# Performance work log

Hardware: AMD Instinct MI355X
Metric: run time of the kernel (lower is better)

The kernel has to match this reference:

```python
import jax, jax.numpy as jnp
import numpy as np

ROUTING_ITERS = 3
EPS = 1e-8

def squash(s):
    # standard CapsNet squash along last axis
    sq = jnp.sum(s * s, axis=-1, keepdims=True)
    return s * (sq / (1.0 + sq)) / jnp.sqrt(sq + EPS)

def setup_inputs() -> dict:
    key = jax.random.key(0)
    k1, k2 = jax.random.split(key)
    B, N_IN, D_IN = 64, 2048, 16
    N_OUT, D_OUT = 32, 32
    x = jax.random.normal(k1, (B, N_IN, D_IN), dtype=jnp.float32)
    kernel = jax.random.normal(k2, (N_IN, N_OUT, D_IN, D_OUT), dtype=jnp.float32) * 0.05
    return {"x": x, "kernel": kernel}

def reference(x, kernel):
    # U[b,n,j,d] = sum_k x[b,n,k] * kernel[n,j,k,d]  (per-input-capsule transform)
    U = jnp.einsum('bnk,njkd->bnjd', x, kernel)
    b, n_in, n_out, _ = U.shape
    Blog = jnp.zeros((b, n_in, n_out), dtype=U.dtype)
    V = None
    for i in range(ROUTING_ITERS):
        C = jax.nn.softmax(Blog, axis=-1)            # [b, n_in, n_out]
        S = jnp.einsum('bnj,bnjd->bjd', C, U)        # weighted sum over input capsules
        V = squash(S)                                # [b, n_out, d_out]
        if i != ROUTING_ITERS - 1:                   # last B update is dead code in original
            Blog = Blog + jnp.einsum('bnjd,bjd->bnj', U, V)
    return V
```

## Files before the change

kernel.cpp:

```cpp
#include <hip/hip_runtime.h>


#define NIN   2048
#define DIN   16
#define NOUT  32
#define DOUT  32
#define NTILE 16
#define NB    (NIN/NTILE)

typedef __attribute__((ext_vector_type(8)))  short s16x8;
typedef __attribute__((ext_vector_type(16))) float f32x16;

#define WS_BLOG   0
#define WS_SPART  4194304
#define WS_SPART2 12582912
#define WS_V      13107200
#define WS_KTF    13172736
#define WS_XTF    29949952

__device__ __forceinline__ unsigned short f2bf(float f) {
  unsigned u = __float_as_uint(f);
  u = (u + 0x7fffu + ((u >> 16) & 1u)) >> 16;
  return (unsigned short)u;
}

__global__ __launch_bounds__(256) void conv_k(const float* __restrict__ Kr,
                                              unsigned short* __restrict__ Ktf) {
  const int n = blockIdx.x;
  const int t = threadIdx.x;
  __shared__ float kl[16384];
  const float* src = Kr + (size_t)n * 16384;
#pragma unroll
  for (int c = 0; c < 16; ++c) {
    const int idx = (c * 256 + t) * 4;
    const int jj  = idx >> 9;
    const int sidx = (idx & ~28) | (((((idx >> 2) & 7) ^ (jj & 7))) << 2);
    *(float4*)&kl[sidx] = *(const float4*)(src + idx);
  }
  __syncthreads();
  unsigned short* dst = Ktf + (size_t)n * 16384;
#pragma unroll
  for (int c = 0; c < 8; ++c) {
    const int chunk = c * 256 + t;
    const int d = chunk >> 6, lane = chunk & 63;
    const int j = lane & 31, khi = lane >> 5;
    const int dsw = ((((d >> 2) ^ (j & 7)) << 2)) | (d & 3);
    unsigned short u8[8];
#pragma unroll
    for (int i = 0; i < 8; ++i)
      u8[i] = f2bf(kl[j * 512 + (khi * 8 + i) * 32 + dsw]);
    uint4 o;
    o.x = u8[0] | ((unsigned)u8[1] << 16);
    o.y = u8[2] | ((unsigned)u8[3] << 16);
    o.z = u8[4] | ((unsigned)u8[5] << 16);
    o.w = u8[6] | ((unsigned)u8[7] << 16);
    *(uint4*)(dst + (size_t)chunk * 8) = o;
  }
}

__global__ __launch_bounds__(256) void conv_x(const float* __restrict__ x,
                                              unsigned short* __restrict__ xtf) {
  const int g = blockIdx.x * 256 + threadIdx.x;
  const int bh = g >> 17, rem = g & 131071;
  const int n = rem >> 6, lane = rem & 63;
  const int b = bh * 32 + (lane & 31), khi = lane >> 5;
  const float* src = x + ((size_t)b * NIN + n) * DIN + khi * 8;
  unsigned short u8[8];
#pragma unroll
  for (int i = 0; i < 8; ++i) u8[i] = f2bf(src[i]);
  uint4 o;
  o.x = u8[0] | ((unsigned)u8[1] << 16);
  o.y = u8[2] | ((unsigned)u8[3] << 16);
  o.z = u8[4] | ((unsigned)u8[5] << 16);
  o.w = u8[6] | ((unsigned)u8[7] << 16);
  *(uint4*)(xtf + (size_t)g * 8) = o;
}

template<int MODE>
__global__ __launch_bounds__(512, 2) void caps_mfma(
    const unsigned short* __restrict__ Ktf, const unsigned short* __restrict__ xtf,
    const float* __restrict__ Vin, float* __restrict__ Blog,
    float* __restrict__ Spart)
{
  const int tid = threadIdx.x;
  const int w = tid >> 6, lane = tid & 63;
  const int j = lane & 31, hi = lane >> 5;
  const int nt = blockIdx.x, bh = blockIdx.y;
  const int n0 = nt * NTILE;

  __shared__ float Ds[8][32][32];
  __shared__ float Cs[32][32];

  float sacc[16][4];
#pragma unroll
  for (int r = 0; r < 16; ++r)
#pragma unroll
    for (int dd = 0; dd < 4; ++dd) sacc[r][dd] = 0.f;

  float vreg[16][4];
  if (MODE != 0) {
#pragma unroll
    for (int r = 0; r < 16; ++r) {
      const int b = (r & 3) + 4 * hi + 8 * (r >> 2);
      const float4 v4 = *(const float4*)(Vin + (((size_t)(bh * 32 + b) * 32 + j) * 32 + w * 4));
      vreg[r][0] = v4.x; vreg[r][1] = v4.y; vreg[r][2] = v4.z; vreg[r][3] = v4.w;
    }
  }

  const int rb = tid >> 5;
  const int rj = tid & 31;

  const unsigned short* xp = xtf + (((size_t)bh * NIN + n0) * 64 + lane) * 8;
  const unsigned short* kp = Ktf + (((size_t)n0 * 32 + w * 4) * 64 + lane) * 8;

  s16x8 a = *(const s16x8*)xp;
  s16x8 bf[4];
#pragma unroll
  for (int dd = 0; dd < 4; ++dd) bf[dd] = *(const s16x8*)(kp + dd * 512);

#pragma unroll 1
  for (int nn = 0; nn < NTILE; ++nn) {
    const int n = n0 + nn;

    f32x16 u[4];
#pragma unroll
    for (int dd = 0; dd < 4; ++dd) {
      f32x16 z;
#pragma unroll
      for (int q = 0; q < 16; ++q) z[q] = 0.f;
      u[dd] = __builtin_amdgcn_mfma_f32_32x32x16_bf16(a, bf[dd], z, 0, 0, 0);
    }

    const int inc = (nn < NTILE - 1) ? 1 : 0;
    const s16x8 a2 = *(const s16x8*)(xp + inc * 512);
    s16x8 bf2[4];
#pragma unroll
    for (int dd = 0; dd < 4; ++dd)
      bf2[dd] = *(const s16x8*)(kp + inc * 16384 + dd * 512);
    xp += inc * 512;
    kp += inc * 16384;

    if (MODE == 0) {
#pragma unroll
      for (int r = 0; r < 16; ++r)
#pragma unroll
        for (int dd = 0; dd < 4; ++dd)
          sacc[r][dd] = fmaf(0.03125f, u[dd][r], sacc[r][dd]);
    } else {
#pragma unroll
      for (int r = 0; r < 16; ++r) {
        const float pd = u[0][r] * vreg[r][0] + u[1][r] * vreg[r][1]
                       + u[2][r] * vreg[r][2] + u[3][r] * vreg[r][3];
        const int b = (r & 3) + 4 * hi + 8 * (r >> 2);
        Ds[w][b][j] = pd;
      }
      __syncthreads();
      float l0 = 0.f, l1 = 0.f;
#pragma unroll
      for (int ww = 0; ww < 8; ++ww) { l0 += Ds[ww][rb][rj]; l1 += Ds[ww][rb + 16][rj]; }
      const size_t bi0 = ((size_t)(bh * 32 + rb) * NIN + n) * 32 + rj;
      const size_t bi1 = ((size_t)(bh * 32 + rb + 16) * NIN + n) * 32 + rj;
      if (MODE == 1) { Blog[bi0] = l0; Blog[bi1] = l1; }
      else           { l0 += Blog[bi0]; l1 += Blog[bi1]; }
      const float e0 = __expf(l0), e1 = __expf(l1);
      float s0 = e0, s1 = e1;
#pragma unroll
      for (int mm = 16; mm >= 1; mm >>= 1) {
        s0 += __shfl_xor(s0, mm, 64);
        s1 += __shfl_xor(s1, mm, 64);
      }
      Cs[rb][rj]      = __fdividef(e0, s0);
      Cs[rb + 16][rj] = __fdividef(e1, s1);
      __syncthreads();
#pragma unroll
      for (int r = 0; r < 16; ++r) {
        const int b = (r & 3) + 4 * hi + 8 * (r >> 2);
        const float c = Cs[b][j];
#pragma unroll
        for (int dd = 0; dd < 4; ++dd) sacc[r][dd] = fmaf(c, u[dd][r], sacc[r][dd]);
      }
    }

    a = a2;
#pragma unroll
    for (int dd = 0; dd < 4; ++dd) bf[dd] = bf2[dd];
  }

  float* Sp = Spart + (size_t)(bh * NB + nt) * 32768;
#pragma unroll
  for (int r = 0; r < 16; ++r) {
    const int b = (r & 3) + 4 * hi + 8 * (r >> 2);
    *(float4*)(Sp + ((size_t)b * 32 + j) * 32 + w * 4) =
        make_float4(sacc[r][0], sacc[r][1], sacc[r][2], sacc[r][3]);
  }
}

__global__ __launch_bounds__(256) void reduce_s1(const float* __restrict__ Spart,
                                                 float* __restrict__ Spart2) {
  const int g = blockIdx.x * 256 + threadIdx.x;
  const int e = g & 65535, p = g >> 16;
  const int bh = e >> 15, ei = e & 32767;
  const float* base = Spart + ((size_t)(bh * NB + p * 16)) * 32768 + ei;
  float s = 0.f;
#pragma unroll
  for (int i = 0; i < 16; ++i) s += base[(size_t)i * 32768];
  Spart2[(size_t)p * 65536 + e] = s;
}

__global__ __launch_bounds__(256) void reduce_s2(const float* __restrict__ Spart2,
                                                 float* __restrict__ Vout) {
  const int t = blockIdx.x * 256 + threadIdx.x;
  float s = 0.f;
#pragma unroll
  for (int p = 0; p < 8; ++p) s += Spart2[(size_t)p * 65536 + t];
  float sq = s * s;
#pragma unroll
  for (int m = 16; m >= 1; m >>= 1) sq += __shfl_xor(sq, m, 64);
  Vout[t] = s * (sq / (1.0f + sq)) * rsqrtf(sq + 1e-8f);
}

extern "C" void kernel_launch(void* const* d_in, const int* in_sizes, int n_in,
                              void* d_out, int out_size, void* d_ws, size_t ws_size,
                              hipStream_t stream) {
  const float* x  = (const float*)d_in[0];
  const float* Kr = (const float*)d_in[1];
  float* ws = (float*)d_ws;
  float* Blog   = ws + WS_BLOG;
  float* Spart  = ws + WS_SPART;
  float* Spart2 = ws + WS_SPART2;
  float* V      = ws + WS_V;
  unsigned short* Ktf = (unsigned short*)(ws + WS_KTF);
  unsigned short* xtf = (unsigned short*)(ws + WS_XTF);
  float* out = (float*)d_out;

  conv_k<<<NIN, 256, 0, stream>>>(Kr, Ktf);
  conv_x<<<1024, 256, 0, stream>>>(x, xtf);

  const dim3 g(NB, 2), blk(512);
  caps_mfma<0><<<g, blk, 0, stream>>>(Ktf, xtf, nullptr, Blog, Spart);
  reduce_s1<<<2048, 256, 0, stream>>>(Spart, Spart2);
  reduce_s2<<<256, 256, 0, stream>>>(Spart2, V);
  caps_mfma<1><<<g, blk, 0, stream>>>(Ktf, xtf, V, Blog, Spart);
  reduce_s1<<<2048, 256, 0, stream>>>(Spart, Spart2);
  reduce_s2<<<256, 256, 0, stream>>>(Spart2, V);
  caps_mfma<2><<<g, blk, 0, stream>>>(Ktf, xtf, V, Blog, Spart);
  reduce_s1<<<2048, 256, 0, stream>>>(Spart, Spart2);
  reduce_s2<<<256, 256, 0, stream>>>(Spart2, out);
}
```

Before: 360.4 us.

## Fuse routing iterations and reductions into one cooperative persistent kernel

Replaces the nine per-iteration launches (three MFMA kernels plus two-stage reductions) with a single cooperative kernel. It loops over the three routing iterations and uses grid-wide syncs to separate the partial-S write from the reduce-and-squash step. This removes launch gaps and the intermediate Spart2 buffer. In exchange, only 64K threads out of 131K do the 128-deep strided reduction, the grid barriers add cost, and the design relies on all 256 blocks of 512 threads being co-resident.

```diff
diff --git a/kernel.cpp b/kernel.cpp
--- a/kernel.cpp
+++ b/kernel.cpp
@@ -1,4 +1,7 @@
 #include <hip/hip_runtime.h>
+#include <hip/hip_cooperative_groups.h>
+
+namespace cg = cooperative_groups;
 
 
 #define NIN   2048
@@ -13,10 +16,9 @@
 
 #define WS_BLOG   0
 #define WS_SPART  4194304
-#define WS_SPART2 12582912
-#define WS_V      13107200
-#define WS_KTF    13172736
-#define WS_XTF    29949952
+#define WS_V      12582912
+#define WS_KTF    12648448
+#define WS_XTF    29425664
 
 __device__ __forceinline__ unsigned short f2bf(float f) {
   unsigned u = __float_as_uint(f);
@@ -76,147 +78,146 @@
   *(uint4*)(xtf + (size_t)g * 8) = o;
 }
 
-template<int MODE>
-__global__ __launch_bounds__(512, 2) void caps_mfma(
+__global__ __launch_bounds__(512, 2) void caps_persist(
     const unsigned short* __restrict__ Ktf, const unsigned short* __restrict__ xtf,
-    const float* __restrict__ Vin, float* __restrict__ Blog,
-    float* __restrict__ Spart)
+    float* __restrict__ Blog, float* __restrict__ Spart,
+    float* __restrict__ Vbuf, float* __restrict__ Out)
 {
+  cg::grid_group grid = cg::this_grid();
   const int tid = threadIdx.x;
   const int w = tid >> 6, lane = tid & 63;
   const int j = lane & 31, hi = lane >> 5;
-  const int nt = blockIdx.x, bh = blockIdx.y;
+  const int blk = blockIdx.x;
+  const int nt = blk & 127, bh = blk >> 7;
   const int n0 = nt * NTILE;
 
   __shared__ float Ds[8][32][32];
   __shared__ float Cs[32][32];
 
-  float sacc[16][4];
-#pragma unroll
-  for (int r = 0; r < 16; ++r)
-#pragma unroll
-    for (int dd = 0; dd < 4; ++dd) sacc[r][dd] = 0.f;
-
-  float vreg[16][4];
-  if (MODE != 0) {
+  const int rb = tid >> 5;
+  const int rj = tid & 31;
+  const int gtid = blk * 512 + tid;
+
+#pragma unroll 1
+  for (int it = 0; it < 3; ++it) {
+    float sacc[16][4];
+#pragma unroll
+    for (int r = 0; r < 16; ++r)
+#pragma unroll
+      for (int dd = 0; dd < 4; ++dd) sacc[r][dd] = 0.f;
+
+    float vreg[16][4];
+    if (it != 0) {
+#pragma unroll
+      for (int r = 0; r < 16; ++r) {
+        const int b = (r & 3) + 4 * hi + 8 * (r >> 2);
+        const float4 v4 = *(const float4*)(Vbuf + (((size_t)(bh * 32 + b) * 32 + j) * 32 + w * 4));
+        vreg[r][0] = v4.x; vreg[r][1] = v4.y; vreg[r][2] = v4.z; vreg[r][3] = v4.w;
+      }
+    }
+
+    const unsigned short* xp = xtf + (((size_t)bh * NIN + n0) * 64 + lane) * 8;
+    const unsigned short* kp = Ktf + (((size_t)n0 * 32 + w * 4) * 64 + lane) * 8;
+
+    s16x8 a = *(const s16x8*)xp;
+    s16x8 bf[4];
+#pragma unroll
+    for (int dd = 0; dd < 4; ++dd) bf[dd] = *(const s16x8*)(kp + dd * 512);
+
+#pragma unroll 1
+    for (int nn = 0; nn < NTILE; ++nn) {
+      const int n = n0 + nn;
+
+      f32x16 u[4];
+#pragma unroll
+      for (int dd = 0; dd < 4; ++dd) {
+        f32x16 z;
+#pragma unroll
+        for (int q = 0; q < 16; ++q) z[q] = 0.f;
+        u[dd] = __builtin_amdgcn_mfma_f32_32x32x16_bf16(a, bf[dd], z, 0, 0, 0);
+      }
+
+      const int inc = (nn < NTILE - 1) ? 1 : 0;
+      const s16x8 a2 = *(const s16x8*)(xp + inc * 512);
+      s16x8 bf2[4];
+#pragma unroll
+      for (int dd = 0; dd < 4; ++dd)
+        bf2[dd] = *(const s16x8*)(kp + inc * 16384 + dd * 512);
+      xp += inc * 512;
+      kp += inc * 16384;
+
+      if (it == 0) {
+#pragma unroll
+        for (int r = 0; r < 16; ++r)
+#pragma unroll
+          for (int dd = 0; dd < 4; ++dd)
+            sacc[r][dd] = fmaf(0.03125f, u[dd][r], sacc[r][dd]);
+      } else {
+#pragma unroll
+        for (int r = 0; r < 16; ++r) {
+          const float pd = u[0][r] * vreg[r][0] + u[1][r] * vreg[r][1]
+                         + u[2][r] * vreg[r][2] + u[3][r] * vreg[r][3];
+          const int b = (r & 3) + 4 * hi + 8 * (r >> 2);
+          Ds[w][b][j] = pd;
+        }
+        __syncthreads();
+        float l0 = 0.f, l1 = 0.f;
+#pragma unroll
+        for (int ww = 0; ww < 8; ++ww) { l0 += Ds[ww][rb][rj]; l1 += Ds[ww][rb + 16][rj]; }
+        const size_t bi0 = ((size_t)(bh * 32 + rb) * NIN + n) * 32 + rj;
+        const size_t bi1 = ((size_t)(bh * 32 + rb + 16) * NIN + n) * 32 + rj;
+        if (it == 1) { Blog[bi0] = l0; Blog[bi1] = l1; }
+        else         { l0 += Blog[bi0]; l1 += Blog[bi1]; }
+        const float e0 = __expf(l0), e1 = __expf(l1);
+        float s0 = e0, s1 = e1;
+#pragma unroll
+        for (int mm = 16; mm >= 1; mm >>= 1) {
+          s0 += __shfl_xor(s0, mm, 64);
+          s1 += __shfl_xor(s1, mm, 64);
+        }
+        Cs[rb][rj]      = __fdividef(e0, s0);
+        Cs[rb + 16][rj] = __fdividef(e1, s1);
+        __syncthreads();
+#pragma unroll
+        for (int r = 0; r < 16; ++r) {
+          const int b = (r & 3) + 4 * hi + 8 * (r >> 2);
+          const float c = Cs[b][j];
+#pragma unroll
+          for (int dd = 0; dd < 4; ++dd) sacc[r][dd] = fmaf(c, u[dd][r], sacc[r][dd]);
+        }
+      }
+
+      a = a2;
+#pragma unroll
+      for (int dd = 0; dd < 4; ++dd) bf[dd] = bf2[dd];
+    }
+
+    float* Sp = Spart + (size_t)blk * 32768;
 #pragma unroll
     for (int r = 0; r < 16; ++r) {
       const int b = (r & 3) + 4 * hi + 8 * (r >> 2);
-      const float4 v4 = *(const float4*)(Vin + (((size_t)(bh * 32 + b) * 32 + j) * 32 + w * 4));
-      vreg[r][0] = v4.x; vreg[r][1] = v4.y; vreg[r][2] = v4.z; vreg[r][3] = v4.w;
-    }
+      *(float4*)(Sp + ((size_t)b * 32 + j) * 32 + w * 4) =
+          make_float4(sacc[r][0], sacc[r][1], sacc[r][2], sacc[r][3]);
+    }
+
+    grid.sync();
+
+    if (gtid < 65536) {
+      const int bhe = gtid >> 15;
+      const int ei  = gtid & 32767;
+      const float* base = Spart + (size_t)(bhe * NB) * 32768 + ei;
+      float s = 0.f;
+#pragma unroll 8
+      for (int t = 0; t < NB; ++t) s += base[(size_t)t * 32768];
+      float sq = s * s;
+#pragma unroll
+      for (int m = 16; m >= 1; m >>= 1) sq += __shfl_xor(sq, m, 64);
+      const float v = s * (sq / (1.0f + sq)) * rsqrtf(sq + 1e-8f);
+      if (it < 2) Vbuf[gtid] = v;
+      else        Out[gtid]  = v;
+    }
+    if (it < 2) grid.sync();
   }
-
-  const int rb = tid >> 5;
-  const int rj = tid & 31;
-
-  const unsigned short* xp = xtf + (((size_t)bh * NIN + n0) * 64 + lane) * 8;
-  const unsigned short* kp = Ktf + (((size_t)n0 * 32 + w * 4) * 64 + lane) * 8;
-
-  s16x8 a = *(const s16x8*)xp;
-  s16x8 bf[4];
-#pragma unroll
-  for (int dd = 0; dd < 4; ++dd) bf[dd] = *(const s16x8*)(kp + dd * 512);
-
-#pragma unroll 1
-  for (int nn = 0; nn < NTILE; ++nn) {
-    const int n = n0 + nn;
-
-    f32x16 u[4];
-#pragma unroll
-    for (int dd = 0; dd < 4; ++dd) {
-      f32x16 z;
-#pragma unroll
-      for (int q = 0; q < 16; ++q) z[q] = 0.f;
-      u[dd] = __builtin_amdgcn_mfma_f32_32x32x16_bf16(a, bf[dd], z, 0, 0, 0);
-    }
-
-    const int inc = (nn < NTILE - 1) ? 1 : 0;
-    const s16x8 a2 = *(const s16x8*)(xp + inc * 512);
-    s16x8 bf2[4];
-#pragma unroll
-    for (int dd = 0; dd < 4; ++dd)
-      bf2[dd] = *(const s16x8*)(kp + inc * 16384 + dd * 512);
-    xp += inc * 512;
-    kp += inc * 16384;
-
-    if (MODE == 0) {
-#pragma unroll
-      for (int r = 0; r < 16; ++r)
-#pragma unroll
-        for (int dd = 0; dd < 4; ++dd)
-          sacc[r][dd] = fmaf(0.03125f, u[dd][r], sacc[r][dd]);
-    } else {
-#pragma unroll
-      for (int r = 0; r < 16; ++r) {
-        const float pd = u[0][r] * vreg[r][0] + u[1][r] * vreg[r][1]
-                       + u[2][r] * vreg[r][2] + u[3][r] * vreg[r][3];
-        const int b = (r & 3) + 4 * hi + 8 * (r >> 2);
-        Ds[w][b][j] = pd;
-      }
-      __syncthreads();
-      float l0 = 0.f, l1 = 0.f;
-#pragma unroll
-      for (int ww = 0; ww < 8; ++ww) { l0 += Ds[ww][rb][rj]; l1 += Ds[ww][rb + 16][rj]; }
-      const size_t bi0 = ((size_t)(bh * 32 + rb) * NIN + n) * 32 + rj;
-      const size_t bi1 = ((size_t)(bh * 32 + rb + 16) * NIN + n) * 32 + rj;
-      if (MODE == 1) { Blog[bi0] = l0; Blog[bi1] = l1; }
-      else           { l0 += Blog[bi0]; l1 += Blog[bi1]; }
-      const float e0 = __expf(l0), e1 = __expf(l1);
-      float s0 = e0, s1 = e1;
-#pragma unroll
-      for (int mm = 16; mm >= 1; mm >>= 1) {
-        s0 += __shfl_xor(s0, mm, 64);
-        s1 += __shfl_xor(s1, mm, 64);
-      }
-      Cs[rb][rj]      = __fdividef(e0, s0);
-      Cs[rb + 16][rj] = __fdividef(e1, s1);
-      __syncthreads();
-#pragma unroll
-      for (int r = 0; r < 16; ++r) {
-        const int b = (r & 3) + 4 * hi + 8 * (r >> 2);
-        const float c = Cs[b][j];
-#pragma unroll
-        for (int dd = 0; dd < 4; ++dd) sacc[r][dd] = fmaf(c, u[dd][r], sacc[r][dd]);
-      }
-    }
-
-    a = a2;
-#pragma unroll
-    for (int dd = 0; dd < 4; ++dd) bf[dd] = bf2[dd];
-  }
-
-  float* Sp = Spart + (size_t)(bh * NB + nt) * 32768;
-#pragma unroll
-  for (int r = 0; r < 16; ++r) {
-    const int b = (r & 3) + 4 * hi + 8 * (r >> 2);
-    *(float4*)(Sp + ((size_t)b * 32 + j) * 32 + w * 4) =
-        make_float4(sacc[r][0], sacc[r][1], sacc[r][2], sacc[r][3]);
-  }
-}
-
-__global__ __launch_bounds__(256) void reduce_s1(const float* __restrict__ Spart,
-                                                 float* __restrict__ Spart2) {
-  const int g = blockIdx.x * 256 + threadIdx.x;
-  const int e = g & 65535, p = g >> 16;
-  const int bh = e >> 15, ei = e & 32767;
-  const float* base = Spart + ((size_t)(bh * NB + p * 16)) * 32768 + ei;
-  float s = 0.f;
-#pragma unroll
-  for (int i = 0; i < 16; ++i) s += base[(size_t)i * 32768];
-  Spart2[(size_t)p * 65536 + e] = s;
-}
-
-__global__ __launch_bounds__(256) void reduce_s2(const float* __restrict__ Spart2,
-                                                 float* __restrict__ Vout) {
-  const int t = blockIdx.x * 256 + threadIdx.x;
-  float s = 0.f;
-#pragma unroll
-  for (int p = 0; p < 8; ++p) s += Spart2[(size_t)p * 65536 + t];
-  float sq = s * s;
-#pragma unroll
-  for (int m = 16; m >= 1; m >>= 1) sq += __shfl_xor(sq, m, 64);
-  Vout[t] = s * (sq / (1.0f + sq)) * rsqrtf(sq + 1e-8f);
 }
 
 extern "C" void kernel_launch(void* const* d_in, const int* in_sizes, int n_in,
@@ -225,10 +226,9 @@
   const float* x  = (const float*)d_in[0];
   const float* Kr = (const float*)d_in[1];
   float* ws = (float*)d_ws;
-  float* Blog   = ws + WS_BLOG;
-  float* Spart  = ws + WS_SPART;
-  float* Spart2 = ws + WS_SPART2;
-  float* V      = ws + WS_V;
+  float* Blog  = ws + WS_BLOG;
+  float* Spart = ws + WS_SPART;
+  float* Vbuf  = ws + WS_V;
   unsigned short* Ktf = (unsigned short*)(ws + WS_KTF);
   unsigned short* xtf = (unsigned short*)(ws + WS_XTF);
   float* out = (float*)d_out;
@@ -236,14 +236,8 @@
   conv_k<<<NIN, 256, 0, stream>>>(Kr, Ktf);
   conv_x<<<1024, 256, 0, stream>>>(x, xtf);
 
-  const dim3 g(NB, 2), blk(512);
-  caps_mfma<0><<<g, blk, 0, stream>>>(Ktf, xtf, nullptr, Blog, Spart);
-  reduce_s1<<<2048, 256, 0, stream>>>(Spart, Spart2);
-  reduce_s2<<<256, 256, 0, stream>>>(Spart2, V);
-  caps_mfma<1><<<g, blk, 0, stream>>>(Ktf, xtf, V, Blog, Spart);
-  reduce_s1<<<2048, 256, 0, stream>>>(Spart, Spart2);
-  reduce_s2<<<256, 256, 0, stream>>>(Spart2, V);
-  caps_mfma<2><<<g, blk, 0, stream>>>(Ktf, xtf, V, Blog, Spart);
-  reduce_s1<<<2048, 256, 0, stream>>>(Spart, Spart2);
-  reduce_s2<<<256, 256, 0, stream>>>(Spart2, out);
-}
+  void* args[] = { (void*)&Ktf, (void*)&xtf, (void*)&Blog, (void*)&Spart,
+                   (void*)&Vbuf, (void*)&out };
+  hipLaunchCooperativeKernel((void*)caps_persist, dim3(256), dim3(512),
+                             args, 0, stream);
+}
```

Measured after the change: 675.5 us. 1.87x slower.

## Double-buffer MODE0 loads, remap block grid for L2 reuse, lighten barriers

Applied to the files above, without the earlier changes.

The MODE 0 kernel now keeps two independent load/MFMA streams (even and odd n), so global loads for one capsule overlap compute on the other. The 2D grid becomes a 1D grid where pairs of batch-halves sharing the same n tiles are adjacent, so both can reuse the same kernel weights from L2. The __syncthreads calls in the routing modes are replaced by a raw LDS waitcnt plus s_barrier with scheduling fences, which avoids waiting on outstanding global prefetches. The changes raise register pressure in MODE 0 and depend on the raw barrier sequence being correct.

```diff
diff --git a/kernel.cpp b/kernel.cpp
--- a/kernel.cpp
+++ b/kernel.cpp
@@ -22,6 +22,13 @@
   unsigned u = __float_as_uint(f);
   u = (u + 0x7fffu + ((u >> 16) & 1u)) >> 16;
   return (unsigned short)u;
+}
+
+__device__ __forceinline__ void lds_barrier() {
+  asm volatile("s_waitcnt lgkmcnt(0)" ::: "memory");
+  __builtin_amdgcn_sched_barrier(0);
+  __builtin_amdgcn_s_barrier();
+  __builtin_amdgcn_sched_barrier(0);
 }
 
 __global__ __launch_bounds__(256) void conv_k(const float* __restrict__ Kr,
@@ -85,7 +92,9 @@
   const int tid = threadIdx.x;
   const int w = tid >> 6, lane = tid & 63;
   const int j = lane & 31, hi = lane >> 5;
-  const int nt = blockIdx.x, bh = blockIdx.y;
+  const int blk = blockIdx.x;
+  const int nt = (blk >> 4) * 8 + (blk & 7);
+  const int bh = (blk >> 3) & 1;
   const int n0 = nt * NTILE;
 
   __shared__ float Ds[8][32][32];
@@ -97,56 +106,105 @@
 #pragma unroll
     for (int dd = 0; dd < 4; ++dd) sacc[r][dd] = 0.f;
 
-  float vreg[16][4];
-  if (MODE != 0) {
+  if (MODE == 0) {
+    const unsigned short* xpA = xtf + (((size_t)bh * NIN + n0) * 64 + lane) * 8;
+    const unsigned short* kpA = Ktf + (((size_t)n0 * 32 + w * 4) * 64 + lane) * 8;
+    const unsigned short* xpB = xpA + 512;
+    const unsigned short* kpB = kpA + 16384;
+
+    s16x8 aA = *(const s16x8*)xpA, aB = *(const s16x8*)xpB;
+    s16x8 bfA[4], bfB[4];
+#pragma unroll
+    for (int dd = 0; dd < 4; ++dd) {
+      bfA[dd] = *(const s16x8*)(kpA + dd * 512);
+      bfB[dd] = *(const s16x8*)(kpB + dd * 512);
+    }
+
+#pragma unroll 1
+    for (int nn = 0; nn < NTILE; nn += 2) {
+      f32x16 u[4];
+#pragma unroll
+      for (int dd = 0; dd < 4; ++dd) {
+        f32x16 z;
+#pragma unroll
+        for (int q = 0; q < 16; ++q) z[q] = 0.f;
+        u[dd] = __builtin_amdgcn_mfma_f32_32x32x16_bf16(aA, bfA[dd], z, 0, 0, 0);
+      }
+      {
+        const int inc = (nn + 2 < NTILE) ? 2 : 0;
+        xpA += inc * 512;  kpA += inc * 16384;
+        aA = *(const s16x8*)xpA;
+#pragma unroll
+        for (int dd = 0; dd < 4; ++dd) bfA[dd] = *(const s16x8*)(kpA + dd * 512);
+      }
+#pragma unroll
+      for (int r = 0; r < 16; ++r)
+#pragma unroll
+        for (int dd = 0; dd < 4; ++dd)
+          sacc[r][dd] = fmaf(0.03125f, u[dd][r], sacc[r][dd]);
+
+#pragma unroll
+      for (int dd = 0; dd < 4; ++dd) {
+        f32x16 z;
+#pragma unroll
+        for (int q = 0; q < 16; ++q) z[q] = 0.f;
+        u[dd] = __builtin_amdgcn_mfma_f32_32x32x16_bf16(aB, bfB[dd], z, 0, 0, 0);
+      }
+      {
+        const int inc = (nn + 3 < NTILE) ? 2 : 0;
+        xpB += inc * 512;  kpB += inc * 16384;
+        aB = *(const s16x8*)xpB;
+#pragma unroll
+        for (int dd = 0; dd < 4; ++dd) bfB[dd] = *(const s16x8*)(kpB + dd * 512);
+      }
+#pragma unroll
+      for (int r = 0; r < 16; ++r)
+#pragma unroll
+        for (int dd = 0; dd < 4; ++dd)
+          sacc[r][dd] = fmaf(0.03125f, u[dd][r], sacc[r][dd]);
+    }
+  } else {
+    float vreg[16][4];
 #pragma unroll
     for (int r = 0; r < 16; ++r) {
       const int b = (r & 3) + 4 * hi + 8 * (r >> 2);
       const float4 v4 = *(const float4*)(Vin + (((size_t)(bh * 32 + b) * 32 + j) * 32 + w * 4));
       vreg[r][0] = v4.x; vreg[r][1] = v4.y; vreg[r][2] = v4.z; vreg[r][3] = v4.w;
     }
-  }
-
-  const int rb = tid >> 5;
-  const int rj = tid & 31;
-
-  const unsigned short* xp = xtf + (((size_t)bh * NIN + n0) * 64 + lane) * 8;
-  const unsigned short* kp = Ktf + (((size_t)n0 * 32 + w * 4) * 64 + lane) * 8;
-
-  s16x8 a = *(const s16x8*)xp;
-  s16x8 bf[4];
-#pragma unroll
-  for (int dd = 0; dd < 4; ++dd) bf[dd] = *(const s16x8*)(kp + dd * 512);
+
+    const int rb = tid >> 5;
+    const int rj = tid & 31;
+
+    const unsigned short* xp = xtf + (((size_t)bh * NIN + n0) * 64 + lane) * 8;
+    const unsigned short* kp = Ktf + (((size_t)n0 * 32 + w * 4) * 64 + lane) * 8;
+
+    s16x8 a = *(const s16x8*)xp;
+    s16x8 bf[4];
+#pragma unroll
+    for (int dd = 0; dd < 4; ++dd) bf[dd] = *(const s16x8*)(kp + dd * 512);
 
 #pragma unroll 1
-  for (int nn = 0; nn < NTILE; ++nn) {
-    const int n = n0 + nn;
-
-    f32x16 u[4];
-#pragma unroll
-    for (int dd = 0; dd < 4; ++dd) {
-      f32x16 z;
-#pragma unroll
-      for (int q = 0; q < 16; ++q) z[q] = 0.f;
-      u[dd] = __builtin_amdgcn_mfma_f32_32x32x16_bf16(a, bf[dd], z, 0, 0, 0);
-    }
-
-    const int inc = (nn < NTILE - 1) ? 1 : 0;
-    const s16x8 a2 = *(const s16x8*)(xp + inc * 512);
-    s16x8 bf2[4];
-#pragma unroll
-    for (int dd = 0; dd < 4; ++dd)
-      bf2[dd] = *(const s16x8*)(kp + inc * 16384 + dd * 512);
-    xp += inc * 512;
-    kp += inc * 16384;
-
-    if (MODE == 0) {
-#pragma unroll
-      for (int r = 0; r < 16; ++r)
-#pragma unroll
-        for (int dd = 0; dd < 4; ++dd)
-          sacc[r][dd] = fmaf(0.03125f, u[dd][r], sacc[r][dd]);
-    } else {
+    for (int nn = 0; nn < NTILE; ++nn) {
+      const int n = n0 + nn;
+
+      f32x16 u[4];
+#pragma unroll
+      for (int dd = 0; dd < 4; ++dd) {
+        f32x16 z;
+#pragma unroll
+        for (int q = 0; q < 16; ++q) z[q] = 0.f;
+        u[dd] = __builtin_amdgcn_mfma_f32_32x32x16_bf16(a, bf[dd], z, 0, 0, 0);
+      }
+
+      const int inc = (nn < NTILE - 1) ? 1 : 0;
+      const s16x8 a2 = *(const s16x8*)(xp + inc * 512);
+      s16x8 bf2[4];
+#pragma unroll
+      for (int dd = 0; dd < 4; ++dd)
+        bf2[dd] = *(const s16x8*)(kp + inc * 16384 + dd * 512);
+      xp += inc * 512;
+      kp += inc * 16384;
+
 #pragma unroll
       for (int r = 0; r < 16; ++r) {
         const float pd = u[0][r] * vreg[r][0] + u[1][r] * vreg[r][1]
@@ -154,7 +212,7 @@
         const int b = (r & 3) + 4 * hi + 8 * (r >> 2);
         Ds[w][b][j] = pd;
       }
-      __syncthreads();
+      lds_barrier();
       float l0 = 0.f, l1 = 0.f;
 #pragma unroll
       for (int ww = 0; ww < 8; ++ww) { l0 += Ds[ww][rb][rj]; l1 += Ds[ww][rb + 16][rj]; }
@@ -171,7 +229,7 @@
       }
       Cs[rb][rj]      = __fdividef(e0, s0);
       Cs[rb + 16][rj] = __fdividef(e1, s1);
-      __syncthreads();
+      lds_barrier();
 #pragma unroll
       for (int r = 0; r < 16; ++r) {
         const int b = (r & 3) + 4 * hi + 8 * (r >> 2);
@@ -179,11 +237,11 @@
 #pragma unroll
         for (int dd = 0; dd < 4; ++dd) sacc[r][dd] = fmaf(c, u[dd][r], sacc[r][dd]);
       }
+
+      a = a2;
+#pragma unroll
+      for (int dd = 0; dd < 4; ++dd) bf[dd] = bf2[dd];
     }
-
-    a = a2;
-#pragma unroll
-    for (int dd = 0; dd < 4; ++dd) bf[dd] = bf2[dd];
   }
 
   float* Sp = Spart + (size_t)(bh * NB + nt) * 32768;
@@ -236,7 +294,7 @@
   conv_k<<<NIN, 256, 0, stream>>>(Kr, Ktf);
   conv_x<<<1024, 256, 0, stream>>>(x, xtf);
 
-  const dim3 g(NB, 2), blk(512);
+  const dim3 g(256), blk(512);
   caps_mfma<0><<<g, blk, 0, stream>>>(Ktf, xtf, nullptr, Blog, Spart);
   reduce_s1<<<2048, 256, 0, stream>>>(Spart, Spart2);
   reduce_s2<<<256, 256, 0, stream>>>(Spart2, V);
```

Measured after the change: 367.8 us. +2.1%, slower.
